# Kernel optimization log

Hardware: AMD Instinct MI355X
Metric: run time of the kernel (lower is better)

## Reference

```python
import jax, jax.numpy as jnp
import numpy as np

N, E = 100000, 1600000
F_IN, H, HG, L, C = 128, 128, 128, 3, 40


def setup_inputs() -> dict:
    key = jax.random.key(0)
    ks = jax.random.split(key, 12)
    s = 0.05
    return dict(
        x=jax.random.normal(ks[0], (N, F_IN), jnp.float32),
        edge_index=jax.random.randint(ks[1], (2, E), 0, N),
        edge_weight=jax.random.uniform(ks[2], (E,), jnp.float32),
        h0=jax.random.normal(ks[3], (N, HG), jnp.float32),
        linW=jax.random.normal(ks[4], (F_IN, H), jnp.float32) * s,
        linB=jnp.zeros((H,), jnp.float32),
        convW=jax.random.normal(ks[5], (L, H, H), jnp.float32) * s,
        convB=jnp.zeros((L, H), jnp.float32),
        gru_Wih=jax.random.normal(ks[6], (3 * HG, H), jnp.float32) * s,
        gru_Whh=jax.random.normal(ks[7], (3 * HG, HG), jnp.float32) * s,
        gru_bih=jnp.zeros((3 * HG,), jnp.float32),
        gru_bhh=jnp.zeros((3 * HG,), jnp.float32),
        fcW=jax.random.normal(ks[8], (HG, C), jnp.float32) * s,
        fcB=jnp.zeros((C,), jnp.float32),
    )


def _gru(x, h, Wih, Whh, bih, bhh):
    # torch.nn.GRUCell math (gate order: r, z, n)
    gi = x @ Wih.T + bih  # [N, 3*HG]
    gh = h @ Whh.T + bhh  # [N, 3*HG]
    ir, iz, in_ = jnp.split(gi, 3, axis=-1)
    hr, hz, hn = jnp.split(gh, 3, axis=-1)
    r = jax.nn.sigmoid(ir + hr)
    z = jax.nn.sigmoid(iz + hz)
    n = jnp.tanh(in_ + r * hn)
    return (1.0 - z) * n + z * h


def _gcn_conv(x, src, dst, ew, W, b, n_nodes):
    # PyG GCNConv: linear -> symmetric-normalized sparse aggregation -> bias
    xw = x @ W  # [N, H]
    deg = jax.ops.segment_sum(ew, dst, num_segments=n_nodes)
    dinv = jnp.where(deg > 0, jax.lax.rsqrt(deg), 0.0)
    norm = dinv[src] * ew * dinv[dst]  # [E+N]
    msg = xw[src] * norm[:, None]      # gather + scale (irregular access)
    out = jax.ops.segment_sum(msg, dst, num_segments=n_nodes)  # scatter-add
    return out + b


def reference(x, edge_index, edge_weight, h0, linW, linB, convW, convB,
              gru_Wih, gru_Whh, gru_bih, gru_bhh, fcW, fcB):
    n_nodes = x.shape[0]
    # GCNConv default: add self-loops with weight 1 before normalization
    loops = jnp.arange(n_nodes)
    src = jnp.concatenate([edge_index[0], loops])
    dst = jnp.concatenate([edge_index[1], loops])
    ew = jnp.concatenate([edge_weight, jnp.ones((n_nodes,), edge_weight.dtype)])

    h = h0
    xh = jax.nn.relu(x @ linW + linB)
    h = _gru(xh, h, gru_Wih, gru_Whh, gru_bih, gru_bhh)
    for l in range(convW.shape[0]):  # fixed small layer count
        xh = jax.nn.relu(_gcn_conv(xh, src, dst, ew, convW[l], convB[l], n_nodes))
        h = _gru(xh, h, gru_Wih, gru_Whh, gru_bih, gru_bhh)
    return h @ fcW + fcB
```

## Files before the change

### kernel.cpp

```cpp
#include <hip/hip_runtime.h>
#include <hip/hip_bf16.h>
#include <math.h>

typedef __attribute__((ext_vector_type(8))) short bf8_t;
typedef __attribute__((ext_vector_type(4))) float f4_t;
typedef __attribute__((ext_vector_type(8))) unsigned short us8_t;

__device__ inline unsigned short f2bf(float f) {
  union { float f; unsigned u; } x; x.f = f;
  unsigned r = x.u + 0x7FFF + ((x.u >> 16) & 1);
  return (unsigned short)(r >> 16);
}
__device__ inline float bflo(unsigned v) {
  union { unsigned u; float f; } x; x.u = v << 16; return x.f;
}
__device__ inline float bfhi(unsigned v) {
  union { unsigned u; float f; } x; x.u = v & 0xFFFF0000u; return x.f;
}
__device__ inline float fast_sig(float x) {
  return __builtin_amdgcn_rcpf(1.f + __expf(-x));
}
__device__ inline float fast_tanh(float x) {
  return 1.f - 2.f * __builtin_amdgcn_rcpf(1.f + __expf(2.f * x));
}

__device__ inline void async_copy16(const void* g, void* l) {
  __builtin_amdgcn_global_load_lds(
      (const __attribute__((address_space(1))) unsigned int*)g,
      (__attribute__((address_space(3))) unsigned int*)l, 16, 0, 0);
}

__device__ inline bf8_t pack_bf8(const float* p) {
  float4 a = *(const float4*)p;
  float4 b = *(const float4*)(p + 4);
  bf8_t t;
  t[0] = (short)f2bf(a.x); t[1] = (short)f2bf(a.y);
  t[2] = (short)f2bf(a.z); t[3] = (short)f2bf(a.w);
  t[4] = (short)f2bf(b.x); t[5] = (short)f2bf(b.y);
  t[6] = (short)f2bf(b.z); t[7] = (short)f2bf(b.w);
  return t;
}


__device__ inline void packB_body(const float* __restrict__ W,
                                  unsigned short* __restrict__ out,
                                  int K, int Ncols, int ldw, int trans, int bid) {
  int idx = bid * 256 + threadIdx.x;
  int total = (Ncols / 16) * (K / 32) * 64;
  if (idx >= total) return;
  int lane = idx & 63;
  int frag = idx >> 6;
  int kt = K / 32;
  int k0 = frag % kt;
  int n0 = frag / kt;
  int n = n0 * 16 + (lane & 15);
  int kbase = k0 * 32 + (lane >> 4) * 8;
  us8_t v;
#pragma unroll
  for (int j = 0; j < 8; ++j) {
    int k = kbase + j;
    float f = trans ? W[(size_t)n * ldw + k] : W[(size_t)k * ldw + n];
    v[j] = f2bf(f);
  }
  *(us8_t*)(out + (size_t)idx * 8) = v;
}

template<bool RELU, bool BIAS, bool F32A>
__device__ inline void gemm_body4(const void* __restrict__ Araw,
                                  const unsigned short* __restrict__ Bp,
                                  const float* __restrict__ bias,
                                  unsigned short* __restrict__ C, int M, int bid,
                                  unsigned char* smem) {
  int wave = threadIdx.x >> 6, lane = threadIdx.x & 63;
  int row0 = (bid * 4 + wave) * 16;
  int m = lane & 15, q = lane >> 4;

#pragma unroll
  for (int i = 0; i < 8; ++i) {
    int f = wave * 8 + i;
    async_copy16((const unsigned char*)Bp + (size_t)f * 1024 + lane * 16,
                 smem + f * 1024);
  }
  __syncthreads();
  if (row0 >= M) return;

  int arow = row0 + m; if (arow >= M) arow = M - 1;
  bf8_t a[4];
#pragma unroll
  for (int k0 = 0; k0 < 4; ++k0) {
    if (F32A) {
      a[k0] = pack_bf8((const float*)Araw + (size_t)arow * 128 + k0 * 32 + q * 8);
    } else {
      a[k0] = *(const bf8_t*)((const unsigned short*)Araw +
                              (size_t)arow * 128 + k0 * 32 + q * 8);
    }
  }

#pragma unroll
  for (int n0 = 0; n0 < 8; ++n0) {
    f4_t acc = {};
#pragma unroll
    for (int k0 = 0; k0 < 4; ++k0) {
      bf8_t b = *(const bf8_t*)(smem + (n0 * 4 + k0) * 1024 + lane * 16);
      acc = __builtin_amdgcn_mfma_f32_16x16x32_bf16(a[k0], b, acc, 0, 0, 0);
    }
    int col = n0 * 16 + m;
    float bs = BIAS ? bias[col] : 0.f;
#pragma unroll
    for (int r = 0; r < 4; ++r) {
      int grow = row0 + q * 4 + r;
      if (grow < M) {
        float v = acc[r] + bs;
        if (RELU) v = fmaxf(v, 0.f);
        C[(size_t)grow * 128 + col] = f2bf(v);
      }
    }
  }
}

__device__ inline void gru_stage4(const unsigned short* __restrict__ Bi,
                                  const unsigned short* __restrict__ Bh,
                                  unsigned char* half, int wave, int lane, int g) {
#pragma unroll
  for (int s = 0; s < 6; ++s) {
    int cc = g + 8 * (s >= 3 ? s - 3 : s);
    const unsigned short* src = (s < 3) ? Bi : Bh;
    int f = s * 4 + wave;
    async_copy16((const unsigned char*)src + ((size_t)(cc * 4 + wave)) * 1024 + lane * 16,
                 half + f * 1024);
  }
}

__device__ inline void gru_core4(const bf8_t* ax, const float* h_in, float* h_out,
                                 const unsigned short* __restrict__ Bi,
                                 const unsigned short* __restrict__ Bh,
                                 const float* __restrict__ bih, const float* __restrict__ bhh,
                                 int M, int row0, int wave, int lane,
                                 unsigned char* smem) {
  int m = lane & 15, q = lane >> 4;
  int arow = row0 + m; if (arow >= M) arow = M - 1;

  bf8_t ah[4];
#pragma unroll
  for (int k0 = 0; k0 < 4; ++k0)
    ah[k0] = pack_bf8(h_in + (size_t)arow * 128 + k0 * 32 + q * 8);

  int erow[4];
#pragma unroll
  for (int r = 0; r < 4; ++r) {
    int gr = row0 + q * 4 + r;
    erow[r] = (gr < M) ? gr : (M - 1);
  }

  float hp_cur[4], hp_nxt[4];
#pragma unroll
  for (int r = 0; r < 4; ++r)
    hp_cur[r] = h_in[(size_t)erow[r] * 128 + m];

#pragma unroll
  for (int g = 0; g < 8; ++g) {
    __syncthreads();
    if (g < 7)
      gru_stage4(Bi, Bh, smem + ((g + 1) & 1) * (24 * 1024), wave, lane, g + 1);
    unsigned char* cur = smem + (g & 1) * (24 * 1024);

    f4_t air = {}, aiz = {}, ain = {}, ahr = {}, ahz = {}, ahn = {};
#pragma unroll
    for (int k0 = 0; k0 < 4; ++k0) {
      bf8_t br = *(const bf8_t*)(cur + (0 * 4 + k0) * 1024 + lane * 16);
      bf8_t bz = *(const bf8_t*)(cur + (1 * 4 + k0) * 1024 + lane * 16);
      bf8_t bn = *(const bf8_t*)(cur + (2 * 4 + k0) * 1024 + lane * 16);
      bf8_t cr = *(const bf8_t*)(cur + (3 * 4 + k0) * 1024 + lane * 16);
      bf8_t cz = *(const bf8_t*)(cur + (4 * 4 + k0) * 1024 + lane * 16);
      bf8_t cn = *(const bf8_t*)(cur + (5 * 4 + k0) * 1024 + lane * 16);
      air = __builtin_amdgcn_mfma_f32_16x16x32_bf16(ax[k0], br, air, 0, 0, 0);
      aiz = __builtin_amdgcn_mfma_f32_16x16x32_bf16(ax[k0], bz, aiz, 0, 0, 0);
      ain = __builtin_amdgcn_mfma_f32_16x16x32_bf16(ax[k0], bn, ain, 0, 0, 0);
      ahr = __builtin_amdgcn_mfma_f32_16x16x32_bf16(ah[k0], cr, ahr, 0, 0, 0);
      ahz = __builtin_amdgcn_mfma_f32_16x16x32_bf16(ah[k0], cz, ahz, 0, 0, 0);
      ahn = __builtin_amdgcn_mfma_f32_16x16x32_bf16(ah[k0], cn, ahn, 0, 0, 0);
    }
    if (g < 7) {
#pragma unroll
      for (int r = 0; r < 4; ++r)
        hp_nxt[r] = h_in[(size_t)erow[r] * 128 + (g + 1) * 16 + m];
    }

    int col = g * 16 + m;
    float bir_ = bih[col], biz_ = bih[col + 128], bin_ = bih[col + 256];
    float bhr_ = bhh[col], bhz_ = bhh[col + 128], bhn_ = bhh[col + 256];
#pragma unroll
    for (int r = 0; r < 4; ++r) {
      int grow = row0 + q * 4 + r;
      if (grow < M) {
        float rr = fast_sig(air[r] + bir_ + ahr[r] + bhr_);
        float zz = fast_sig(aiz[r] + biz_ + ahz[r] + bhz_);
        float nn = fast_tanh(ain[r] + bin_ + rr * (ahn[r] + bhn_));
        h_out[(size_t)grow * 128 + col] = (1.f - zz) * nn + zz * hp_cur[r];
      }
    }
#pragma unroll
    for (int r = 0; r < 4; ++r) hp_cur[r] = hp_nxt[r];
  }
}


__global__ __launch_bounds__(256) void k_prep(
    const float* __restrict__ linW, const float* __restrict__ convW,
    const float* __restrict__ Wih, const float* __restrict__ Whh,
    unsigned short* __restrict__ linWp, unsigned short* __restrict__ convWp,
    unsigned short* __restrict__ Bi, unsigned short* __restrict__ Bh,
    int* __restrict__ cnt, int N) {
  int b = blockIdx.x;
  if (b < 8)  { packB_body(linW, linWp, 128, 128, 128, 0, b); return; }
  if (b < 32) { int l = (b - 8) >> 3;
                packB_body(convW + (size_t)l * 16384, convWp + (size_t)l * 16384,
                           128, 128, 128, 0, (b - 8) & 7); return; }
  if (b < 56) { packB_body(Wih, Bi, 128, 384, 128, 1, b - 32); return; }
  if (b < 80) { packB_body(Whh, Bh, 128, 384, 128, 1, b - 56); return; }
  int i = (b - 80) * 256 + threadIdx.x;
  if (i < N) cnt[i] = 0;
}

__global__ __launch_bounds__(256) void k_count_lin(
    const int* __restrict__ dst, int* __restrict__ cnt, int* __restrict__ pos, int E,
    const float* __restrict__ x, const unsigned short* __restrict__ linWp,
    const float* __restrict__ linB, unsigned short* __restrict__ xh, int M,
    int nCnt) {
  __shared__ unsigned char smem[32 * 1024];
  if ((int)blockIdx.x < nCnt) {
    int e = blockIdx.x * 256 + threadIdx.x;
    if (e < E) pos[e] = atomicAdd(&cnt[dst[e]], 1);
    return;
  }
  gemm_body4<true, true, true>(x, linWp, linB, xh, M, blockIdx.x - nCnt, smem);
}

__global__ __launch_bounds__(256) void k_scan_block(
    const int* __restrict__ cnt, int* __restrict__ partial,
    int* __restrict__ bsum, int n) {
  __shared__ int s[256];
  int tid = threadIdx.x;
  int i = blockIdx.x * 256 + tid;
  s[tid] = (i < n) ? cnt[i] : 0;
  __syncthreads();
#pragma unroll
  for (int d = 1; d < 256; d <<= 1) {
    int t = (tid >= d) ? s[tid - d] : 0;
    __syncthreads();
    s[tid] += t;
    __syncthreads();
  }
  if (i < n) partial[i] = s[tid];
  if (tid == 255) bsum[blockIdx.x] = s[255];
}

__global__ __launch_bounds__(256) void k_scan_add(
    const int* __restrict__ partial, const int* __restrict__ bsum,
    int* __restrict__ rowptr, int n, int nb) {
  __shared__ int s[512];
  int tid = threadIdx.x;
  s[tid] = (tid < nb) ? bsum[tid] : 0;
  s[tid + 256] = (tid + 256 < nb) ? bsum[tid + 256] : 0;
  __syncthreads();
#pragma unroll
  for (int d = 1; d < 512; d <<= 1) {
    int t0 = (tid >= d) ? s[tid - d] : 0;
    int t1 = (tid + 256 >= d) ? s[tid + 256 - d] : 0;
    __syncthreads();
    s[tid] += t0;
    s[tid + 256] += t1;
    __syncthreads();
  }
  int base = (blockIdx.x > 0) ? s[blockIdx.x - 1] : 0;
  int i = blockIdx.x * 256 + tid;
  if (i == 0) rowptr[0] = 0;
  if (i < n) rowptr[i + 1] = partial[i] + base;
}

__global__ __launch_bounds__(512) void k_fill(
    const int* __restrict__ src, const int* __restrict__ dst,
    const float* __restrict__ ew, const int* __restrict__ rowptr,
    const int* __restrict__ pos, int2* __restrict__ csr, int E) {
  int e = blockIdx.x * 512 + threadIdx.x;
  if (e >= E) return;
  int d = dst[e];
  int p = rowptr[d] + pos[e];
  unsigned long long v = (unsigned long long)(unsigned)src[e] |
                         ((unsigned long long)(unsigned)__float_as_int(ew[e]) << 32);
  __builtin_nontemporal_store(v, (unsigned long long*)(csr + p));
}

__global__ __launch_bounds__(512) void k_deg(
    const int* __restrict__ rowptr, const int2* __restrict__ csr,
    float* __restrict__ dinv, int N) {
  int n = blockIdx.x * 512 + threadIdx.x;
  if (n >= N) return;
  int b = rowptr[n], e = rowptr[n + 1];
  float s = 1.0f;
  for (int j = b; j < e; ++j) {
    unsigned long long v = __builtin_nontemporal_load((const unsigned long long*)(csr + j));
    s += __int_as_float((int)(v >> 32));
  }
  dinv[n] = rsqrtf(s);
}

__global__ __launch_bounds__(256) void k_conv(
    const unsigned short* __restrict__ A, const unsigned short* __restrict__ Bp,
    unsigned short* __restrict__ C, int M) {
  __shared__ unsigned char smem[32 * 1024];
  gemm_body4<false, false, false>(A, Bp, nullptr, C, M, blockIdx.x, smem);
}

__global__ __launch_bounds__(256, 3) void k_gru(
    const unsigned short* __restrict__ xh, const float* h_in, float* h_out,
    const unsigned short* __restrict__ Bi, const unsigned short* __restrict__ Bh,
    const float* __restrict__ bih, const float* __restrict__ bhh, int M) {
  __shared__ unsigned char smem[2 * 24 * 1024];
  int wave = threadIdx.x >> 6, lane = threadIdx.x & 63;
  int row0 = (blockIdx.x * 4 + wave) * 16;
  gru_stage4(Bi, Bh, smem, wave, lane, 0);
  int m = lane & 15, q = lane >> 4;
  int arow = row0 + m; if (arow >= M) arow = M - 1;
  bf8_t ax[4];
#pragma unroll
  for (int k0 = 0; k0 < 4; ++k0)
    ax[k0] = *(const bf8_t*)(xh + (size_t)arow * 128 + k0 * 32 + q * 8);
  gru_core4(ax, h_in, h_out, Bi, Bh, bih, bhh, M, row0, wave, lane, smem);
}


__global__ __launch_bounds__(256) void k_gather(
    const int* __restrict__ rowptr, const int2* __restrict__ csr,
    const unsigned* __restrict__ xw,
    const float* __restrict__ dinv, const float* __restrict__ bias,
    unsigned* __restrict__ out, int N) {
  int wave = threadIdx.x >> 6;
  int lane = threadIdx.x & 63;
  int node = __builtin_amdgcn_readfirstlane(blockIdx.x * 4 + wave);
  if (node >= N) return;
  int beg = __builtin_amdgcn_readfirstlane(rowptr[node]);
  int end = __builtin_amdgcn_readfirstlane(rowptr[node + 1]);
  float di = dinv[node];

  float accl = 0.f, acch = 0.f;
  int k = beg;
  for (; k + 4 <= end; k += 4) {
    unsigned long long r0 = __builtin_nontemporal_load((const unsigned long long*)(csr + k));
    unsigned long long r1 = __builtin_nontemporal_load((const unsigned long long*)(csr + k + 1));
    unsigned long long r2 = __builtin_nontemporal_load((const unsigned long long*)(csr + k + 2));
    unsigned long long r3 = __builtin_nontemporal_load((const unsigned long long*)(csr + k + 3));
    unsigned v0 = xw[((size_t)(unsigned)r0 << 6) + lane];
    unsigned v1 = xw[((size_t)(unsigned)r1 << 6) + lane];
    unsigned v2 = xw[((size_t)(unsigned)r2 << 6) + lane];
    unsigned v3 = xw[((size_t)(unsigned)r3 << 6) + lane];
    float w0 = dinv[(unsigned)r0] * __int_as_float((int)(r0 >> 32)) * di;
    float w1 = dinv[(unsigned)r1] * __int_as_float((int)(r1 >> 32)) * di;
    float w2 = dinv[(unsigned)r2] * __int_as_float((int)(r2 >> 32)) * di;
    float w3 = dinv[(unsigned)r3] * __int_as_float((int)(r3 >> 32)) * di;
    accl += bflo(v0) * w0; acch += bfhi(v0) * w0;
    accl += bflo(v1) * w1; acch += bfhi(v1) * w1;
    accl += bflo(v2) * w2; acch += bfhi(v2) * w2;
    accl += bflo(v3) * w3; acch += bfhi(v3) * w3;
  }
  for (; k < end; ++k) {
    unsigned long long r = __builtin_nontemporal_load((const unsigned long long*)(csr + k));
    unsigned v = xw[((size_t)(unsigned)r << 6) + lane];
    float w = dinv[(unsigned)r] * __int_as_float((int)(r >> 32)) * di;
    accl += bflo(v) * w; acch += bfhi(v) * w;
  }

  float sn = di * di;
  unsigned vs = xw[((size_t)node << 6) + lane];
  float2 b = *(const float2*)(bias + lane * 2);
  float rl = fmaxf(accl + bflo(vs) * sn + b.x, 0.f);
  float rh = fmaxf(acch + bfhi(vs) * sn + b.y, 0.f);
  unsigned o = (unsigned)f2bf(rl) | ((unsigned)f2bf(rh) << 16);
  out[((size_t)node << 6) + lane] = o;
}


template<bool RELU, bool BIAS>
__global__ __launch_bounds__(256) void k_gemm128(
    const float* __restrict__ A, const float* __restrict__ B,
    const float* __restrict__ bias, float* __restrict__ C, int M, int Nc) {
  __shared__ float As[64][36];
  __shared__ float Bs[32][64];
  int tid = threadIdx.x;
  int tx = tid & 15, ty = tid >> 4;
  int row0 = blockIdx.y * 64, col0 = blockIdx.x * 64;
  float acc[4][4] = {};

  for (int k0 = 0; k0 < 128; k0 += 32) {
#pragma unroll
    for (int i = 0; i < 2; ++i) {
      int f = tid + i * 256;
      int r = f >> 3, c4 = f & 7;
      int gr = row0 + r;
      float4 v = make_float4(0.f, 0.f, 0.f, 0.f);
      if (gr < M) v = *(const float4*)(A + (size_t)gr * 128 + k0 + c4 * 4);
      *(float4*)(&As[r][c4 * 4]) = v;
    }
#pragma unroll
    for (int i = 0; i < 2; ++i) {
      int f = tid + i * 256;
      int r = f >> 4, c4 = f & 15;
      int gc = col0 + c4 * 4;
      float4 v = make_float4(0.f, 0.f, 0.f, 0.f);
      if (gc + 3 < Nc) v = *(const float4*)(B + (size_t)(k0 + r) * Nc + gc);
      *(float4*)(&Bs[r][c4 * 4]) = v;
    }
    __syncthreads();
#pragma unroll
    for (int kk = 0; kk < 32; ++kk) {
      float4 b = *(float4*)(&Bs[kk][tx * 4]);
      float a0 = As[ty * 4 + 0][kk];
      float a1 = As[ty * 4 + 1][kk];
      float a2 = As[ty * 4 + 2][kk];
      float a3 = As[ty * 4 + 3][kk];
      acc[0][0] += a0 * b.x; acc[0][1] += a0 * b.y; acc[0][2] += a0 * b.z; acc[0][3] += a0 * b.w;
      acc[1][0] += a1 * b.x; acc[1][1] += a1 * b.y; acc[1][2] += a1 * b.z; acc[1][3] += a1 * b.w;
      acc[2][0] += a2 * b.x; acc[2][1] += a2 * b.y; acc[2][2] += a2 * b.z; acc[2][3] += a2 * b.w;
      acc[3][0] += a3 * b.x; acc[3][1] += a3 * b.y; acc[3][2] += a3 * b.z; acc[3][3] += a3 * b.w;
    }
    __syncthreads();
  }

#pragma unroll
  for (int i = 0; i < 4; ++i) {
    int gr = row0 + ty * 4 + i;
    if (gr >= M) continue;
#pragma unroll
    for (int j = 0; j < 4; ++j) {
      int gc = col0 + tx * 4 + j;
      if (gc >= Nc) continue;
      float v = acc[i][j];
      if (BIAS) v += bias[gc];
      if (RELU) v = fmaxf(v, 0.f);
      C[(size_t)gr * Nc + gc] = v;
    }
  }
}


extern "C" void kernel_launch(void* const* d_in, const int* in_sizes, int n_in,
                              void* d_out, int out_size, void* d_ws, size_t ws_size,
                              hipStream_t stream) {
  const float* x    = (const float*)d_in[0];
  const int*   ei   = (const int*)d_in[1];
  const float* ew   = (const float*)d_in[2];
  const float* h0   = (const float*)d_in[3];
  const float* linW = (const float*)d_in[4];
  const float* linB = (const float*)d_in[5];
  const float* convW= (const float*)d_in[6];
  const float* convB= (const float*)d_in[7];
  const float* Wih  = (const float*)d_in[8];
  const float* Whh  = (const float*)d_in[9];
  const float* bih  = (const float*)d_in[10];
  const float* bhh  = (const float*)d_in[11];
  const float* fcW  = (const float*)d_in[12];
  const float* fcB  = (const float*)d_in[13];

  int N = in_sizes[0] / 128;
  int E = in_sizes[1] / 2;
  const int* srcI = ei;
  const int* dstI = ei + E;
  int nb = (N + 255) / 256;

  float* ws = (float*)d_ws;
  size_t off = 0;
  float* dinv = ws + off; off += (size_t)N;
  if (off & 1) off++;
  float* h    = ws + off; off += (size_t)N * 128;
  int* iws = (int*)(ws + off);
  size_t ioff = 0;
  int2* csr    = (int2*)iws; ioff += (size_t)2 * E;
  int* cnt     = iws + ioff; ioff += (size_t)N;
  int* partial = iws + ioff; ioff += (size_t)N;
  int* bsum    = iws + ioff; ioff += 512;
  int* rowptr  = iws + ioff; ioff += (size_t)N + 1;
  ioff = (ioff + 3) & ~(size_t)3;
  unsigned short* usws = (unsigned short*)(iws + ioff);
  size_t uoff = 0;
  unsigned short* xh_bf  = usws + uoff; uoff += (size_t)N * 128;
  unsigned short* xw_bf  = usws + uoff; uoff += (size_t)N * 128;
  unsigned short* linWp  = usws + uoff; uoff += 128 * 128;
  unsigned short* convWp = usws + uoff; uoff += 3 * 128 * 128;
  unsigned short* Bi     = usws + uoff; uoff += 384 * 128;
  unsigned short* Bh     = usws + uoff; uoff += 384 * 128;

  int* pos = (int*)xw_bf;

  int gw4  = (N + 63) / 64;
  int nCnt = (E + 255) / 256;
  int n512 = (N + 511) / 512;
  int e512 = (E + 511) / 512;
  int ggat = (N + 3) / 4;

  k_prep<<<80 + nb, 256, 0, stream>>>(linW, convW, Wih, Whh,
                                      linWp, convWp, Bi, Bh, cnt, N);
  k_count_lin<<<nCnt + gw4, 256, 0, stream>>>(dstI, cnt, pos, E,
                                              x, linWp, linB, xh_bf, N, nCnt);
  k_scan_block<<<nb, 256, 0, stream>>>(cnt, partial, bsum, N);
  k_scan_add<<<nb, 256, 0, stream>>>(partial, bsum, rowptr, N, nb);
  k_fill<<<e512, 512, 0, stream>>>(srcI, dstI, ew, rowptr, pos, csr, E);
  k_deg<<<n512, 512, 0, stream>>>(rowptr, csr, dinv, N);
  k_gru<<<gw4, 256, 0, stream>>>(xh_bf, h0, h, Bi, Bh, bih, bhh, N);
  for (int l = 0; l < 3; ++l) {
    k_conv<<<gw4, 256, 0, stream>>>(
        xh_bf, convWp + (size_t)l * 128 * 128, xw_bf, N);
    k_gather<<<ggat, 256, 0, stream>>>(
        rowptr, csr, (const unsigned*)xw_bf, dinv, convB + (size_t)l * 128,
        (unsigned*)xh_bf, N);
    k_gru<<<gw4, 256, 0, stream>>>(xh_bf, h, h, Bi, Bh, bih, bhh, N);
  }
  dim3 g40(1, (N + 63) / 64);
  k_gemm128<false, true><<<g40, 256, 0, stream>>>(h, fcW, fcB, (float*)d_out, N, 40);
}
```

Before: 868.5 us.

## Split edge counting across linear and first GRU kernels; unroll gather by eight

```diff
diff --git a/kernel.cpp b/kernel.cpp
--- a/kernel.cpp
+++ b/kernel.cpp
@@ -202,6 +202,24 @@
 #pragma unroll
     for (int r = 0; r < 4; ++r) hp_cur[r] = hp_nxt[r];
   }
+}
+
+__device__ inline void gru_body4(const unsigned short* __restrict__ xh,
+                                 const float* h_in, float* h_out,
+                                 const unsigned short* __restrict__ Bi,
+                                 const unsigned short* __restrict__ Bh,
+                                 const float* __restrict__ bih, const float* __restrict__ bhh,
+                                 int M, int bid, unsigned char* smem) {
+  int wave = threadIdx.x >> 6, lane = threadIdx.x & 63;
+  int row0 = (bid * 4 + wave) * 16;
+  gru_stage4(Bi, Bh, smem, wave, lane, 0);
+  int m = lane & 15, q = lane >> 4;
+  int arow = row0 + m; if (arow >= M) arow = M - 1;
+  bf8_t ax[4];
+#pragma unroll
+  for (int k0 = 0; k0 < 4; ++k0)
+    ax[k0] = *(const bf8_t*)(xh + (size_t)arow * 128 + k0 * 32 + q * 8);
+  gru_core4(ax, h_in, h_out, Bi, Bh, bih, bhh, M, row0, wave, lane, smem);
 }
 
 
@@ -223,17 +241,33 @@
 }
 
 __global__ __launch_bounds__(256) void k_count_lin(
-    const int* __restrict__ dst, int* __restrict__ cnt, int* __restrict__ pos, int E,
+    const int* __restrict__ dst, int* __restrict__ cnt, int* __restrict__ pos,
+    int E2,
     const float* __restrict__ x, const unsigned short* __restrict__ linWp,
     const float* __restrict__ linB, unsigned short* __restrict__ xh, int M,
     int nCnt) {
   __shared__ unsigned char smem[32 * 1024];
   if ((int)blockIdx.x < nCnt) {
     int e = blockIdx.x * 256 + threadIdx.x;
-    if (e < E) pos[e] = atomicAdd(&cnt[dst[e]], 1);
+    if (e < E2) pos[e] = atomicAdd(&cnt[dst[e]], 1);
     return;
   }
   gemm_body4<true, true, true>(x, linWp, linB, xh, M, blockIdx.x - nCnt, smem);
+}
+
+__global__ __launch_bounds__(256, 3) void k_count_gru(
+    const unsigned short* __restrict__ xh, const float* h_in, float* h_out,
+    const unsigned short* __restrict__ Bi, const unsigned short* __restrict__ Bh,
+    const float* __restrict__ bih, const float* __restrict__ bhh, int M,
+    const int* __restrict__ dst, int* __restrict__ cnt, int* __restrict__ pos,
+    int E2, int E, int nGru) {
+  __shared__ unsigned char smem[2 * 24 * 1024];
+  if ((int)blockIdx.x < nGru) {
+    gru_body4(xh, h_in, h_out, Bi, Bh, bih, bhh, M, blockIdx.x, smem);
+    return;
+  }
+  int e = E2 + (blockIdx.x - nGru) * 256 + threadIdx.x;
+  if (e < E) pos[e] = atomicAdd(&cnt[dst[e]], 1);
 }
 
 __global__ __launch_bounds__(256) void k_scan_block(
@@ -317,16 +351,7 @@
     const unsigned short* __restrict__ Bi, const unsigned short* __restrict__ Bh,
     const float* __restrict__ bih, const float* __restrict__ bhh, int M) {
   __shared__ unsigned char smem[2 * 24 * 1024];
-  int wave = threadIdx.x >> 6, lane = threadIdx.x & 63;
-  int row0 = (blockIdx.x * 4 + wave) * 16;
-  gru_stage4(Bi, Bh, smem, wave, lane, 0);
-  int m = lane & 15, q = lane >> 4;
-  int arow = row0 + m; if (arow >= M) arow = M - 1;
-  bf8_t ax[4];
-#pragma unroll
-  for (int k0 = 0; k0 < 4; ++k0)
-    ax[k0] = *(const bf8_t*)(xh + (size_t)arow * 128 + k0 * 32 + q * 8);
-  gru_core4(ax, h_in, h_out, Bi, Bh, bih, bhh, M, row0, wave, lane, smem);
+  gru_body4(xh, h_in, h_out, Bi, Bh, bih, bhh, M, blockIdx.x, smem);
 }
 
 
@@ -345,6 +370,40 @@
 
   float accl = 0.f, acch = 0.f;
   int k = beg;
+  for (; k + 8 <= end; k += 8) {
+    unsigned long long r0 = __builtin_nontemporal_load((const unsigned long long*)(csr + k));
+    unsigned long long r1 = __builtin_nontemporal_load((const unsigned long long*)(csr + k + 1));
+    unsigned long long r2 = __builtin_nontemporal_load((const unsigned long long*)(csr + k + 2));
+    unsigned long long r3 = __builtin_nontemporal_load((const unsigned long long*)(csr + k + 3));
+    unsigned long long r4 = __builtin_nontemporal_load((const unsigned long long*)(csr + k + 4));
+    unsigned long long r5 = __builtin_nontemporal_load((const unsigned long long*)(csr + k + 5));
+    unsigned long long r6 = __builtin_nontemporal_load((const unsigned long long*)(csr + k + 6));
+    unsigned long long r7 = __builtin_nontemporal_load((const unsigned long long*)(csr + k + 7));
+    unsigned v0 = xw[((size_t)(unsigned)r0 << 6) + lane];
+    unsigned v1 = xw[((size_t)(unsigned)r1 << 6) + lane];
+    unsigned v2 = xw[((size_t)(unsigned)r2 << 6) + lane];
+    unsigned v3 = xw[((size_t)(unsigned)r3 << 6) + lane];
+    unsigned v4 = xw[((size_t)(unsigned)r4 << 6) + lane];
+    unsigned v5 = xw[((size_t)(unsigned)r5 << 6) + lane];
+    unsigned v6 = xw[((size_t)(unsigned)r6 << 6) + lane];
+    unsigned v7 = xw[((size_t)(unsigned)r7 << 6) + lane];
+    float w0 = dinv[(unsigned)r0] * __int_as_float((int)(r0 >> 32)) * di;
+    float w1 = dinv[(unsigned)r1] * __int_as_float((int)(r1 >> 32)) * di;
+    float w2 = dinv[(unsigned)r2] * __int_as_float((int)(r2 >> 32)) * di;
+    float w3 = dinv[(unsigned)r3] * __int_as_float((int)(r3 >> 32)) * di;
+    float w4 = dinv[(unsigned)r4] * __int_as_float((int)(r4 >> 32)) * di;
+    float w5 = dinv[(unsigned)r5] * __int_as_float((int)(r5 >> 32)) * di;
+    float w6 = dinv[(unsigned)r6] * __int_as_float((int)(r6 >> 32)) * di;
+    float w7 = dinv[(unsigned)r7] * __int_as_float((int)(r7 >> 32)) * di;
+    accl += bflo(v0) * w0; acch += bfhi(v0) * w0;
+    accl += bflo(v1) * w1; acch += bfhi(v1) * w1;
+    accl += bflo(v2) * w2; acch += bfhi(v2) * w2;
+    accl += bflo(v3) * w3; acch += bfhi(v3) * w3;
+    accl += bflo(v4) * w4; acch += bfhi(v4) * w4;
+    accl += bflo(v5) * w5; acch += bfhi(v5) * w5;
+    accl += bflo(v6) * w6; acch += bfhi(v6) * w6;
+    accl += bflo(v7) * w7; acch += bfhi(v7) * w7;
+  }
   for (; k + 4 <= end; k += 4) {
     unsigned long long r0 = __builtin_nontemporal_load((const unsigned long long*)(csr + k));
     unsigned long long r1 = __builtin_nontemporal_load((const unsigned long long*)(csr + k + 1));
@@ -492,20 +551,25 @@
   int* pos = (int*)xw_bf;
 
   int gw4  = (N + 63) / 64;
-  int nCnt = (E + 255) / 256;
+  int E2   = ((E / 2 + 255) / 256) * 256;
+  if (E2 > E) E2 = E;
+  int nCnt1 = E2 / 256;
+  int nCnt2 = (E - E2 + 255) / 256;
   int n512 = (N + 511) / 512;
   int e512 = (E + 511) / 512;
   int ggat = (N + 3) / 4;
 
   k_prep<<<80 + nb, 256, 0, stream>>>(linW, convW, Wih, Whh,
                                       linWp, convWp, Bi, Bh, cnt, N);
-  k_count_lin<<<nCnt + gw4, 256, 0, stream>>>(dstI, cnt, pos, E,
-                                              x, linWp, linB, xh_bf, N, nCnt);
+  k_count_lin<<<nCnt1 + gw4, 256, 0, stream>>>(dstI, cnt, pos, E2,
+                                               x, linWp, linB, xh_bf, N, nCnt1);
+  k_count_gru<<<gw4 + nCnt2, 256, 0, stream>>>(
+      xh_bf, h0, h, Bi, Bh, bih, bhh, N,
+      dstI, cnt, pos, E2, E, gw4);
   k_scan_block<<<nb, 256, 0, stream>>>(cnt, partial, bsum, N);
   k_scan_add<<<nb, 256, 0, stream>>>(partial, bsum, rowptr, N, nb);
   k_fill<<<e512, 512, 0, stream>>>(srcI, dstI, ew, rowptr, pos, csr, E);
   k_deg<<<n512, 512, 0, stream>>>(rowptr, csr, dinv, N);
-  k_gru<<<gw4, 256, 0, stream>>>(xh_bf, h0, h, Bi, Bh, bih, bhh, N);
   for (int l = 0; l < 3; ++l) {
     k_conv<<<gw4, 256, 0, stream>>>(
         xh_bf, convWp + (size_t)l * 128 * 128, xw_bf, N);
```

Measured after the change: 1.020 ms. +17.4%, slower.
